# Performance work log

Measured on AMD Instinct MI355X. Metric: run time of the kernel, lower is better.

## Reference

```python
import jax, jax.numpy as jnp
import numpy as np

N, M, ND, K = 80000, 150000, 10000, 27  # active voxels, 2D painted points, downscaled voxels, 3x3x3 kernel
C3, C2, CP = 16, 64, 259                # 3D ch (stage 1), 2D conv ch, painted 2D feature ch
CM, CO = C3 + C2, 32 + 64               # mixed ch (80), downscale out ch (96)


def subm_conv(feats, nbr, W):
    """Submanifold sparse conv as gather + per-offset GEMM.
    feats: [N_in, Cin], nbr: [N_out, K] int (-1 = missing), W: [K, Cin, Cout]."""
    out = jnp.zeros((nbr.shape[0], W.shape[-1]), feats.dtype)
    for k in range(W.shape[0]):  # fixed small kernel loop (27)
        idx = nbr[:, k]
        g = jnp.where((idx >= 0)[:, None], feats[jnp.clip(idx, 0)], 0.0)
        out = out + g @ W[k]
    return out


def bn_relu(x, gamma, beta):  # folded eval-mode BN1d + ReLU
    return jax.nn.relu(x * gamma + beta)


def setup_inputs() -> dict:
    key = jax.random.key(0)
    ks = jax.random.split(key, 24)

    def w(k, shape, fan_in):
        return jax.random.normal(k, shape, jnp.float32) * (1.0 / np.sqrt(fan_in))

    inp = {
        'x3d': jax.random.normal(ks[0], (N, C3), jnp.float32),
        'f2d': jax.random.normal(ks[1], (M, CP), jnp.float32),
        'nn_idx': jax.random.randint(ks[2], (N,), -1, M, jnp.int32),     # -1 = no 2D match
        'nbr': jax.random.randint(ks[3], (N, K), -1, N, jnp.int32),      # -1 = missing neighbor
        'nbr_ds': jax.random.randint(ks[4], (ND, K), -1, N, jnp.int32),
        'W3d': w(ks[5], (K, C3, C3), K * C3),
        'g3d': jnp.ones((C3,), jnp.float32), 'b3d': jnp.zeros((C3,), jnp.float32),
        'Wg': w(ks[6], (C3, CP), C3), 'bg': jnp.zeros((CP,), jnp.float32),
        'Wc': w(ks[7], (C3, CP), C3), 'bc': jnp.zeros((CP,), jnp.float32),
        'Wp': w(ks[8], (CP, C2), CP),
        'W2d': w(ks[9], (K, C2, C2), K * C2),
        'g2d': jnp.ones((C2,), jnp.float32), 'b2d': jnp.zeros((C2,), jnp.float32),
        'Wm1': w(ks[10], (K, CM, CM), K * CM),
        'gm1': jnp.ones((CM,), jnp.float32), 'bm1': jnp.zeros((CM,), jnp.float32),
        'Wm2': w(ks[11], (K, CM, CM), K * CM),
        'gm2': jnp.ones((CM,), jnp.float32), 'bm2': jnp.zeros((CM,), jnp.float32),
        'Wa1': w(ks[12], (K, CM, CM), K * CM),
        'ga1': jnp.ones((CM,), jnp.float32), 'ba1': jnp.zeros((CM,), jnp.float32),
        'Wa2': w(ks[13], (K, CM, CM), K * CM),
        'ga2': jnp.ones((CM,), jnp.float32), 'ba2': jnp.zeros((CM,), jnp.float32),
        'Wds': w(ks[14], (K, CM, CO), K * CM),
        'gds': jnp.ones((CO,), jnp.float32), 'bds': jnp.zeros((CO,), jnp.float32),
    }
    return inp


def reference(x3d, f2d, nn_idx, nbr, nbr_ds,
              W3d, g3d, b3d, Wg, bg, Wc, bc, Wp,
              W2d, g2d, b2d,
              Wm1, gm1, bm1, Wm2, gm2, bm2,
              Wa1, ga1, ba1, Wa2, ga2, ba2,
              Wds, gds, bds):
    # irregular gather of painted 2D features to voxel sites (NN index, -1 invalid)
    f2g = jnp.where((nn_idx >= 0)[:, None], f2d[jnp.clip(nn_idx, 0)], 0.0)  # [N, 259]

    # 3D branch: SubMConv3d(C3->C3) + BN + ReLU
    y3d = bn_relu(subm_conv(x3d, nbr, W3d), g3d, b3d)                       # [N, 16]

    # per-stage gate / cross-gate (Linear + ReLU) on 3D features, applied to raw 2D feats
    gate = jax.nn.relu(y3d @ Wg + bg)                                       # [N, 259]
    cross = jax.nn.relu(y3d @ Wc + bc)                                      # [N, 259]

    # gated 2D branch: project gated painted feats to 64, SubMConv3d + BN + ReLU
    p2d = (gate * f2g) @ Wp                                                 # [N, 64]
    x2d = bn_relu(subm_conv(p2d, nbr, W2d), g2d, b2d)                       # [N, 64]
    cross2d = (cross * f2g) @ Wp                                            # [N, 64]

    # cross-modal mix + SparseBasicBlock (residual, two subm convs)
    mix = jnp.concatenate([y3d, x2d + cross2d], axis=-1)                    # [N, 80]
    h = bn_relu(subm_conv(mix, nbr, Wm1), gm1, bm1)
    h = jax.nn.relu(subm_conv(h, nbr, Wm2) * gm2 + bm2 + mix)

    # aggregation SparseBasicBlock
    a = bn_relu(subm_conv(h, nbr, Wa1), ga1, ba1)
    a = jax.nn.relu(subm_conv(a, nbr, Wa2) * ga2 + ba2 + h)

    # strided SparseConv3d downscale (gather from input sites at new out sites)
    out = bn_relu(subm_conv(a, nbr_ds, Wds), gds, bds)                      # [ND, 96]
    return out
```

## Files before the change

### kernel.cpp

```cpp
#include <hip/hip_runtime.h>

#define NPTS 80000
#define MPTS 150000
#define NDPTS 10000
#define KOFF 27
#define C3 16
#define CP 259
#define C2 64
#define CM 80
#define CO 96

typedef __attribute__((ext_vector_type(8))) short short8;
typedef __attribute__((ext_vector_type(4))) float f32x4;

__device__ inline short bf16r(float f) {
  union { float f; unsigned u; } x{f};
  unsigned r = (x.u + 0x7fffu + ((x.u >> 16) & 1u)) >> 16;
  return (short)r;
}

__global__ void wfrag_kernel(const float* __restrict__ W, short* __restrict__ WbfF,
                             int CIN, int COUT_, int KC) {
  const int NT = COUT_ / 16;
  int i = blockIdx.x * 256 + threadIdx.x;
  int total = KOFF * KC * NT * 512;
  if (i >= total) return;
  int j = i & 7, lane = (i >> 3) & 63;
  int rest = i >> 9;
  int t = rest % NT; rest /= NT;
  int q = rest % KC;
  int k = rest / KC;
  int ci = q * 32 + (lane >> 4) * 8 + j;
  int n = t * 16 + (lane & 15);
  float v = (ci < CIN) ? W[((size_t)k * CIN + ci) * COUT_ + n] : 0.f;
  WbfF[i] = bf16r(v);
}

__global__ void wpfrag_kernel(const float* __restrict__ Wp, short* __restrict__ WpF) {
  int i = blockIdx.x * 256 + threadIdx.x;
  if (i >= 9 * 4 * 64 * 8) return;
  int j = i & 7, lane = (i >> 3) & 63, t = (i >> 9) & 3, q = i >> 11;
  int k = q * 32 + (lane >> 4) * 8 + j;
  int n = t * 16 + (lane & 15);
  WpF[i] = (k < CP) ? bf16r(Wp[(size_t)k * C2 + n]) : (short)0;
}

__global__ __launch_bounds__(256) void conv3d_bnrelu_kernel(
    const float* __restrict__ x3d, const int* __restrict__ nbr,
    const float* __restrict__ W3d, const float* __restrict__ g3d,
    const float* __restrict__ b3d, float* __restrict__ y3d,
    float* __restrict__ mix, short* __restrict__ mixbf)
{
  __shared__ float wS[KOFF * C3 * C3];
  __shared__ float fS[16][C3];
  const int tid = threadIdx.x;
  const int base = blockIdx.x * 16;
  for (int e = tid; e < KOFF * C3 * C3; e += 256) wS[e] = W3d[e];
  const int r = tid >> 4, c = tid & 15;
  const int row = base + r;
  float acc = 0.f;
  for (int k = 0; k < KOFF; ++k) {
    int idx = nbr[row * KOFF + k];
    float fv = (idx >= 0) ? x3d[idx * C3 + c] : 0.f;
    __syncthreads();
    fS[r][c] = fv;
    __syncthreads();
    const float* wk = &wS[k * C3 * C3];
    #pragma unroll
    for (int ci = 0; ci < C3; ++ci)
      acc = fmaf(fS[r][ci], wk[ci * C3 + c], acc);
  }
  float v = fmaxf(fmaf(acc, g3d[c], b3d[c]), 0.f);
  y3d[row * C3 + c] = v;
  mix[row * CM + c] = v;
  mixbf[row * CM + c] = bf16r(v);
}

__global__ __launch_bounds__(256) void gate_cross_mfma_kernel(
    const float* __restrict__ y3d, const float* __restrict__ f2d,
    const int* __restrict__ nn_idx,
    const float* __restrict__ Wg, const float* __restrict__ bg,
    const float* __restrict__ Wc, const float* __restrict__ bc,
    const short* __restrict__ WpF,
    short* __restrict__ p2dbf, float* __restrict__ cross2d)
{
  constexpr int RS = 296;
  __shared__ short g1S[32 * RS];
  __shared__ short g2S[32 * RS];
  __shared__ float yS[32][C3];
  const int tid = threadIdx.x;
  const int lane = tid & 63;
  const int w = tid >> 6;
  const int lm = lane & 15;
  const int quad = lane >> 4;
  const int base = blockIdx.x * 32;

  for (int e = tid; e < 32 * 32; e += 256) {
    int r = e >> 5, cc = 256 + (e & 31);
    if (cc >= CP) {
      g1S[r * RS + cc] = 0;
      g2S[r * RS + cc] = 0;
    }
  }

  int ix[32];
  #pragma unroll
  for (int r = 0; r < 32; ++r) ix[r] = nn_idx[base + r];

  const int c = tid;
  float f[32];
  #pragma unroll
  for (int r = 0; r < 32; ++r)
    f[r] = (ix[r] >= 0) ? f2d[(size_t)ix[r] * CP + c] : 0.f;

  float ftail = 0.f;
  int tr = 0, tcc = 0;
  if (tid < 96) {
    tr = tid / 3; tcc = tid - tr * 3;
    if (ix[tr] >= 0) ftail = f2d[(size_t)ix[tr] * CP + 256 + tcc];
  }

  for (int e = tid; e < 32 * C3; e += 256)
    ((float*)yS)[e] = y3d[(size_t)base * C3 + e];

  float wg[16], wc[16];
  #pragma unroll
  for (int ci = 0; ci < 16; ++ci) {
    wg[ci] = Wg[ci * CP + c];
    wc[ci] = Wc[ci * CP + c];
  }
  const float bgv = bg[c], bcv = bc[c];

  __syncthreads();

  #pragma unroll
  for (int r = 0; r < 32; ++r) {
    float a1 = bgv, a2 = bcv;
    #pragma unroll
    for (int ci = 0; ci < 16; ++ci) {
      float yv = yS[r][ci];
      a1 = fmaf(yv, wg[ci], a1);
      a2 = fmaf(yv, wc[ci], a2);
    }
    g1S[r * RS + c] = bf16r(fmaxf(a1, 0.f) * f[r]);
    g2S[r * RS + c] = bf16r(fmaxf(a2, 0.f) * f[r]);
  }

  if (tid < 96) {
    const int c2 = 256 + tcc;
    float a1 = bg[c2], a2 = bc[c2];
    #pragma unroll
    for (int ci = 0; ci < 16; ++ci) {
      float yv = yS[tr][ci];
      a1 = fmaf(yv, Wg[ci * CP + c2], a1);
      a2 = fmaf(yv, Wc[ci * CP + c2], a2);
    }
    g1S[tr * RS + c2] = bf16r(fmaxf(a1, 0.f) * ftail);
    g2S[tr * RS + c2] = bf16r(fmaxf(a2, 0.f) * ftail);
  }
  __syncthreads();

  const int gsel = w & 1;
  const int mt = w >> 1;
  const short* gS = gsel ? g2S : g1S;
  f32x4 acc[4];
  #pragma unroll
  for (int t = 0; t < 4; ++t) {
    f32x4 z = {0.f, 0.f, 0.f, 0.f};
    acc[t] = z;
  }
  #pragma unroll
  for (int q = 0; q < 9; ++q) {
    short8 af = *(const short8*)&gS[(mt * 16 + lm) * RS + q * 32 + quad * 8];
    #pragma unroll
    for (int t = 0; t < 4; ++t) {
      short8 bf = *(const short8*)&WpF[(((q * 4 + t) * 64) + lane) * 8];
      acc[t] = __builtin_amdgcn_mfma_f32_16x16x32_bf16(af, bf, acc[t], 0, 0, 0);
    }
  }
  #pragma unroll
  for (int t = 0; t < 4; ++t) {
    const int cc = t * 16 + lm;
    #pragma unroll
    for (int rg = 0; rg < 4; ++rg) {
      const int row = base + mt * 16 + quad * 4 + rg;
      float v = acc[t][rg];
      if (gsel == 0)
        p2dbf[(size_t)row * C2 + cc] = bf16r(v);
      else
        cross2d[(size_t)row * C2 + cc] = v;
    }
  }
}

template <int CIN, int COUT_, int MODE, int MT>
__global__ __launch_bounds__(64, 2) void conv_nolds_kernel(
    const short* __restrict__ finbf, const int* __restrict__ nbr, int nrows,
    const short* __restrict__ WbfF, const float* __restrict__ gamma,
    const float* __restrict__ beta, const float* __restrict__ resf,
    float* __restrict__ outf, short* __restrict__ outbf)
{
  constexpr int KC = (CIN + 31) / 32;
  constexpr int DCH = CIN / 8;
  constexpr int NT = COUT_ / 16;

  const int lane = threadIdx.x;
  const int lm = lane & 15;
  const int quad = lane >> 4;
  const int base = blockIdx.x * (MT * 16);

  int rrow[MT];
  bool rok[MT];
  #pragma unroll
  for (int i = 0; i < MT; ++i) {
    rrow[i] = base + i * 16 + lm;
    rok[i] = rrow[i] < nrows;
  }

  f32x4 acc[MT][NT];
  #pragma unroll
  for (int i = 0; i < MT; ++i)
    #pragma unroll
    for (int t = 0; t < NT; ++t) {
      f32x4 z = {0.f, 0.f, 0.f, 0.f};
      acc[i][t] = z;
    }

  const short8 zero8 = {0, 0, 0, 0, 0, 0, 0, 0};

  auto loadIdx = [&](int (&id)[MT], int k) {
    #pragma unroll
    for (int i = 0; i < MT; ++i)
      id[i] = (k < KOFF && rok[i]) ? nbr[(size_t)rrow[i] * KOFF + k] : -1;
  };

  auto loadA = [&](short8 (&pa)[MT][KC], const int (&id)[MT]) {
    #pragma unroll
    for (int i = 0; i < MT; ++i) {
      const int safe = (id[i] < 0) ? 0 : id[i];
      const bool ok = id[i] >= 0;
      const short* src = finbf + (size_t)safe * CIN;
      #pragma unroll
      for (int q = 0; q < KC; ++q) {
        const int ch = q * 4 + quad;
        short8 v = zero8;
        if (ch < DCH) v = *(const short8*)(src + ch * 8);
        pa[i][q] = ok ? v : zero8;
      }
    }
  };

  auto computeK = [&](const short8 (&pa)[MT][KC], int k) {
    const short* wb = WbfF + ((size_t)k * KC * NT) * 512 + lane * 8;
    #pragma unroll
    for (int q = 0; q < KC; ++q) {
      #pragma unroll
      for (int t = 0; t < NT; ++t) {
        short8 bfr = *(const short8*)(wb + (q * NT + t) * 512);
        #pragma unroll
        for (int i = 0; i < MT; ++i)
          acc[i][t] = __builtin_amdgcn_mfma_f32_16x16x32_bf16(pa[i][q], bfr,
                                                              acc[i][t], 0, 0, 0);
      }
    }
  };

  int ia[MT], ib[MT], ic[MT];
  short8 paA[MT][KC], paB[MT][KC], paC[MT][KC];

  loadIdx(ia, 0); loadIdx(ib, 1); loadIdx(ic, 2);
  loadA(paA, ia); loadIdx(ia, 3);
  loadA(paB, ib); loadIdx(ib, 4);

  for (int kk = 0; kk < KOFF; kk += 3) {
    loadA(paC, ic); loadIdx(ic, kk + 5);
    computeK(paA, kk);
    loadA(paA, ia); loadIdx(ia, kk + 6);
    computeK(paB, kk + 1);
    loadA(paB, ib); loadIdx(ib, kk + 7);
    computeK(paC, kk + 2);
  }

  #pragma unroll
  for (int i = 0; i < MT; ++i) {
    int rbase = base + i * 16 + quad * 4;
    #pragma unroll
    for (int t = 0; t < NT; ++t) {
      int cc = t * 16 + lm;
      float g = gamma[cc], b = beta[cc];
      #pragma unroll
      for (int rg = 0; rg < 4; ++rg) {
        int row = rbase + rg;
        if (row >= nrows) continue;
        float v = acc[i][t][rg];
        if (MODE == 0) {
          outf[(size_t)row * COUT_ + cc] = fmaxf(fmaf(v, g, b), 0.f);
        } else if (MODE == 1) {
          outbf[(size_t)row * COUT_ + cc] = bf16r(fmaxf(fmaf(v, g, b), 0.f));
        } else if (MODE == 2) {
          float o = fmaxf(fmaf(v, g, b), 0.f) + resf[(size_t)row * C2 + cc];
          outf[(size_t)row * CM + 16 + cc] = o;
          outbf[(size_t)row * CM + 16 + cc] = bf16r(o);
        } else if (MODE == 3) {
          float o = fmaxf(fmaf(v, g, b) + resf[(size_t)row * COUT_ + cc], 0.f);
          outf[(size_t)row * COUT_ + cc] = o;
          outbf[(size_t)row * COUT_ + cc] = bf16r(o);
        } else {
          float o = fmaxf(fmaf(v, g, b) + resf[(size_t)row * COUT_ + cc], 0.f);
          outbf[(size_t)row * COUT_ + cc] = bf16r(o);
        }
      }
    }
  }
}

extern "C" void kernel_launch(void* const* d_in, const int* in_sizes, int n_in,
                              void* d_out, int out_size, void* d_ws, size_t ws_size,
                              hipStream_t stream) {
  const float* x3d  = (const float*)d_in[0];
  const float* f2d  = (const float*)d_in[1];
  const int*   nn   = (const int*)d_in[2];
  const int*   nbr  = (const int*)d_in[3];
  const int*   nbds = (const int*)d_in[4];
  const float* W3d  = (const float*)d_in[5];
  const float* g3d  = (const float*)d_in[6];
  const float* b3d  = (const float*)d_in[7];
  const float* Wg   = (const float*)d_in[8];
  const float* bg   = (const float*)d_in[9];
  const float* Wc   = (const float*)d_in[10];
  const float* bc   = (const float*)d_in[11];
  const float* Wp   = (const float*)d_in[12];
  const float* W2d  = (const float*)d_in[13];
  const float* g2d  = (const float*)d_in[14];
  const float* b2d  = (const float*)d_in[15];
  const float* Wm1  = (const float*)d_in[16];
  const float* gm1  = (const float*)d_in[17];
  const float* bm1  = (const float*)d_in[18];
  const float* Wm2  = (const float*)d_in[19];
  const float* gm2  = (const float*)d_in[20];
  const float* bm2  = (const float*)d_in[21];
  const float* Wa1  = (const float*)d_in[22];
  const float* ga1  = (const float*)d_in[23];
  const float* ba1  = (const float*)d_in[24];
  const float* Wa2  = (const float*)d_in[25];
  const float* ga2  = (const float*)d_in[26];
  const float* ba2  = (const float*)d_in[27];
  const float* Wds  = (const float*)d_in[28];
  const float* gds  = (const float*)d_in[29];
  const float* bds  = (const float*)d_in[30];

  const size_t N = NPTS;
  float* ws = (float*)d_ws;
  float* y3d     = ws;
  short* p2dbf   = (short*)(ws + N * 16);
  float* cross2d = ws + N * 48;
  float* mix     = ws + N * 112;
  short* mixbf   = (short*)(ws + N * 192);
  short* tmp1bf  = (short*)(ws + N * 232);
  float* hbuf    = ws + N * 272;
  short* hbufbf  = (short*)(ws + N * 352);
  short* abufbf  = (short*)ws;
  short* wtail  = (short*)(ws + N * 392);
  short* WbfF2d = wtail;
  short* WbfFm1 = WbfF2d + 110592;
  short* WbfFm2 = WbfFm1 + 207360;
  short* WbfFa1 = WbfFm2 + 207360;
  short* WbfFa2 = WbfFa1 + 207360;
  short* WbfFds = WbfFa2 + 207360;
  short* WpF    = WbfFds + 248832;

  wfrag_kernel<<<(110592 + 255) / 256, 256, 0, stream>>>(W2d, WbfF2d, 64, 64, 2);
  wfrag_kernel<<<(207360 + 255) / 256, 256, 0, stream>>>(Wm1, WbfFm1, 80, 80, 3);
  wfrag_kernel<<<(207360 + 255) / 256, 256, 0, stream>>>(Wm2, WbfFm2, 80, 80, 3);
  wfrag_kernel<<<(207360 + 255) / 256, 256, 0, stream>>>(Wa1, WbfFa1, 80, 80, 3);
  wfrag_kernel<<<(207360 + 255) / 256, 256, 0, stream>>>(Wa2, WbfFa2, 80, 80, 3);
  wfrag_kernel<<<(248832 + 255) / 256, 256, 0, stream>>>(Wds, WbfFds, 80, 96, 3);
  wpfrag_kernel<<<(9 * 4 * 64 * 8 + 255) / 256, 256, 0, stream>>>(Wp, WpF);

  conv3d_bnrelu_kernel<<<NPTS / 16, 256, 0, stream>>>(x3d, nbr, W3d, g3d, b3d,
                                                      y3d, mix, mixbf);
  gate_cross_mfma_kernel<<<NPTS / 32, 256, 0, stream>>>(y3d, f2d, nn, Wg, bg,
                                                        Wc, bc, WpF, p2dbf,
                                                        cross2d);

  const int gridM2 = (NPTS + 31) / 32;
  const int gridM4 = (NPTS + 63) / 64;
  conv_nolds_kernel<64, 64, 2, 2><<<gridM2, 64, 0, stream>>>(
      p2dbf, nbr, NPTS, WbfF2d, g2d, b2d, cross2d, mix, mixbf);
  conv_nolds_kernel<80, 80, 1, 2><<<gridM2, 64, 0, stream>>>(
      mixbf, nbr, NPTS, WbfFm1, gm1, bm1, nullptr, nullptr, tmp1bf);
  conv_nolds_kernel<80, 80, 3, 4><<<gridM4, 64, 0, stream>>>(
      tmp1bf, nbr, NPTS, WbfFm2, gm2, bm2, mix, hbuf, hbufbf);
  conv_nolds_kernel<80, 80, 1, 2><<<gridM2, 64, 0, stream>>>(
      hbufbf, nbr, NPTS, WbfFa1, ga1, ba1, nullptr, nullptr, tmp1bf);
  conv_nolds_kernel<80, 80, 4, 2><<<gridM2, 64, 0, stream>>>(
      tmp1bf, nbr, NPTS, WbfFa2, ga2, ba2, hbuf, nullptr, abufbf);

  const int gridDS = (NDPTS + 31) / 32;
  conv_nolds_kernel<80, 96, 0, 2><<<gridDS, 64, 0, stream>>>(
      abufbf, nbds, NDPTS, WbfFds, gds, bds, nullptr, (float*)d_out, nullptr);
}
```

Measured before the change: 1.161 ms.

## Stage sparse-conv gathers and weights into LDS via async global_load_lds double buffering

Replaces the register-prefetch sparse conv kernel with one that preloads the block's neighbor indices into shared memory and streams gathered feature rows and weight fragments into double-buffered LDS using global_load_lds, synchronised with manual vmcnt waits. The goal is to hide gather latency behind MFMA work and cut register pressure without tying up VGPRs for prefetched fragments. The tile is fixed at 32 rows (the MT=4 variant is dropped) and launch bounds change to one block per SIMD hint. The hand-coded vmcnt thresholds are brittle and depend on the exact number of outstanding loads, and the launch bounds limit occupancy.

```diff
diff --git a/kernel.cpp b/kernel.cpp
--- a/kernel.cpp
+++ b/kernel.cpp
@@ -17,6 +17,12 @@
   union { float f; unsigned u; } x{f};
   unsigned r = (x.u + 0x7fffu + ((x.u >> 16) & 1u)) >> 16;
   return (short)r;
+}
+
+typedef __attribute__((address_space(1))) const unsigned int g_u32;
+typedef __attribute__((address_space(3))) unsigned int l_u32;
+__device__ __forceinline__ void gload_lds16(const void* g, void* l) {
+  __builtin_amdgcn_global_load_lds((g_u32*)g, (l_u32*)l, 16, 0, 0);
 }
 
 __global__ void wfrag_kernel(const float* __restrict__ W, short* __restrict__ WbfF,
@@ -193,8 +199,8 @@
   }
 }
 
-template <int CIN, int COUT_, int MODE, int MT>
-__global__ __launch_bounds__(64, 2) void conv_nolds_kernel(
+template <int CIN, int COUT_, int MODE>
+__global__ __launch_bounds__(64, 1) void conv_glds_kernel(
     const short* __restrict__ finbf, const int* __restrict__ nbr, int nrows,
     const short* __restrict__ WbfF, const float* __restrict__ gamma,
     const float* __restrict__ beta, const float* __restrict__ resf,
@@ -203,18 +209,22 @@
   constexpr int KC = (CIN + 31) / 32;
   constexpr int DCH = CIN / 8;
   constexpr int NT = COUT_ / 16;
+  constexpr int MT = 2;
+  constexpr int WN = MT * KC + KC * NT;
+
+  __shared__ short8 aS[2 * MT * KC * 64];
+  __shared__ short8 bS[2 * KC * NT * 64];
+  __shared__ int nbrS[32 * KOFF];
 
   const int lane = threadIdx.x;
   const int lm = lane & 15;
   const int quad = lane >> 4;
-  const int base = blockIdx.x * (MT * 16);
-
-  int rrow[MT];
-  bool rok[MT];
-  #pragma unroll
-  for (int i = 0; i < MT; ++i) {
-    rrow[i] = base + i * 16 + lm;
-    rok[i] = rrow[i] < nrows;
+  const int base = blockIdx.x * 32;
+
+  for (int e = lane; e < 32 * KOFF; e += 64) {
+    int r = e / KOFF;
+    int row = base + r;
+    nbrS[e] = (row < nrows) ? nbr[(size_t)row * KOFF + (e - r * KOFF)] : -1;
   }
 
   f32x4 acc[MT][NT];
@@ -226,59 +236,125 @@
       acc[i][t] = z;
     }
 
-  const short8 zero8 = {0, 0, 0, 0, 0, 0, 0, 0};
-
-  auto loadIdx = [&](int (&id)[MT], int k) {
+  auto readIdx = [&](int k, int (&id)[MT]) {
     #pragma unroll
     for (int i = 0; i < MT; ++i)
-      id[i] = (k < KOFF && rok[i]) ? nbr[(size_t)rrow[i] * KOFF + k] : -1;
+      id[i] = (k < KOFF) ? nbrS[(i * 16 + lm) * KOFF + k] : -1;
   };
 
-  auto loadA = [&](short8 (&pa)[MT][KC], const int (&id)[MT]) {
+  auto stage = [&](int k2, const int (&id)[MT]) {
+    const int slot = k2 & 1;
     #pragma unroll
     for (int i = 0; i < MT; ++i) {
       const int safe = (id[i] < 0) ? 0 : id[i];
-      const bool ok = id[i] >= 0;
-      const short* src = finbf + (size_t)safe * CIN;
+      const short* srow = finbf + (size_t)safe * CIN;
       #pragma unroll
       for (int q = 0; q < KC; ++q) {
         const int ch = q * 4 + quad;
-        short8 v = zero8;
-        if (ch < DCH) v = *(const short8*)(src + ch * 8);
-        pa[i][q] = ok ? v : zero8;
+        const int chs = (ch < DCH) ? ch : (DCH - 1);
+        gload_lds16(srow + chs * 8, &aS[((slot * MT + i) * KC + q) * 64]);
       }
     }
+    const short* wb = WbfF + (size_t)k2 * (KC * NT * 512) + lane * 8;
+    #pragma unroll
+    for (int q = 0; q < KC; ++q)
+      #pragma unroll
+      for (int t = 0; t < NT; ++t)
+        gload_lds16(wb + (q * NT + t) * 512, &bS[((slot * KC + q) * NT + t) * 64]);
   };
 
-  auto computeK = [&](const short8 (&pa)[MT][KC], int k) {
-    const short* wb = WbfF + ((size_t)k * KC * NT) * 512 + lane * 8;
-    #pragma unroll
-    for (int q = 0; q < KC; ++q) {
-      #pragma unroll
-      for (int t = 0; t < NT; ++t) {
-        short8 bfr = *(const short8*)(wb + (q * NT + t) * 512);
+  auto waitSlot = [&]() {
+    if constexpr (WN == 12)      asm volatile("s_waitcnt vmcnt(12)" ::: "memory");
+    else if constexpr (WN == 21) asm volatile("s_waitcnt vmcnt(21)" ::: "memory");
+    else                         asm volatile("s_waitcnt vmcnt(24)" ::: "memory");
+  };
+
+  const short8 zero8 = {0, 0, 0, 0, 0, 0, 0, 0};
+
+  {
+    int id0[MT], id1[MT];
+    readIdx(0, id0);
+    readIdx(1, id1);
+    stage(0, id0);
+    stage(1, id1);
+  }
+
+  for (int k = 0; k < KOFF - 1; ++k) {
+    const int slot = k & 1;
+    waitSlot();
+    short8 va[MT][KC];
+    #pragma unroll
+    for (int i = 0; i < MT; ++i)
+      #pragma unroll
+      for (int q = 0; q < KC; ++q)
+        va[i][q] = aS[((slot * MT + i) * KC + q) * 64 + lane];
+    short8 vb[KC][NT];
+    #pragma unroll
+    for (int q = 0; q < KC; ++q)
+      #pragma unroll
+      for (int t = 0; t < NT; ++t)
+        vb[q][t] = bS[((slot * KC + q) * NT + t) * 64 + lane];
+    int ikc[MT], ikn[MT];
+    readIdx(k, ikc);
+    readIdx(k + 2, ikn);
+    asm volatile("s_waitcnt lgkmcnt(0)" ::: "memory");
+    __builtin_amdgcn_sched_barrier(0);
+    #pragma unroll
+    for (int i = 0; i < MT; ++i) {
+      const bool okr = ikc[i] >= 0;
+      #pragma unroll
+      for (int q = 0; q < KC; ++q) {
+        const bool okc = okr && ((q * 4 + quad) < DCH);
+        va[i][q] = okc ? va[i][q] : zero8;
+      }
+    }
+    if (k + 2 < KOFF) stage(k + 2, ikn);
+    #pragma unroll
+    for (int q = 0; q < KC; ++q)
+      #pragma unroll
+      for (int t = 0; t < NT; ++t)
         #pragma unroll
         for (int i = 0; i < MT; ++i)
-          acc[i][t] = __builtin_amdgcn_mfma_f32_16x16x32_bf16(pa[i][q], bfr,
+          acc[i][t] = __builtin_amdgcn_mfma_f32_16x16x32_bf16(va[i][q], vb[q][t],
                                                               acc[i][t], 0, 0, 0);
+  }
+  {
+    const int k = KOFF - 1;
+    const int slot = k & 1;
+    asm volatile("s_waitcnt vmcnt(0)" ::: "memory");
+    short8 va[MT][KC];
+    #pragma unroll
+    for (int i = 0; i < MT; ++i)
+      #pragma unroll
+      for (int q = 0; q < KC; ++q)
+        va[i][q] = aS[((slot * MT + i) * KC + q) * 64 + lane];
+    short8 vb[KC][NT];
+    #pragma unroll
+    for (int q = 0; q < KC; ++q)
+      #pragma unroll
+      for (int t = 0; t < NT; ++t)
+        vb[q][t] = bS[((slot * KC + q) * NT + t) * 64 + lane];
+    int ikc[MT];
+    readIdx(k, ikc);
+    asm volatile("s_waitcnt lgkmcnt(0)" ::: "memory");
+    __builtin_amdgcn_sched_barrier(0);
+    #pragma unroll
+    for (int i = 0; i < MT; ++i) {
+      const bool okr = ikc[i] >= 0;
+      #pragma unroll
+      for (int q = 0; q < KC; ++q) {
+        const bool okc = okr && ((q * 4 + quad) < DCH);
+        va[i][q] = okc ? va[i][q] : zero8;
       }
     }
-  };
-
-  int ia[MT], ib[MT], ic[MT];
-  short8 paA[MT][KC], paB[MT][KC], paC[MT][KC];
-
-  loadIdx(ia, 0); loadIdx(ib, 1); loadIdx(ic, 2);
-  loadA(paA, ia); loadIdx(ia, 3);
-  loadA(paB, ib); loadIdx(ib, 4);
-
-  for (int kk = 0; kk < KOFF; kk += 3) {
-    loadA(paC, ic); loadIdx(ic, kk + 5);
-    computeK(paA, kk);
-    loadA(paA, ia); loadIdx(ia, kk + 6);
-    computeK(paB, kk + 1);
-    loadA(paB, ib); loadIdx(ib, kk + 7);
-    computeK(paC, kk + 2);
+    #pragma unroll
+    for (int q = 0; q < KC; ++q)
+      #pragma unroll
+      for (int t = 0; t < NT; ++t)
+        #pragma unroll
+        for (int i = 0; i < MT; ++i)
+          acc[i][t] = __builtin_amdgcn_mfma_f32_16x16x32_bf16(va[i][q], vb[q][t],
+                                                              acc[i][t], 0, 0, 0);
   }
 
   #pragma unroll
@@ -383,20 +459,19 @@
                                                         Wc, bc, WpF, p2dbf,
                                                         cross2d);
 
-  const int gridM2 = (NPTS + 31) / 32;
-  const int gridM4 = (NPTS + 63) / 64;
-  conv_nolds_kernel<64, 64, 2, 2><<<gridM2, 64, 0, stream>>>(
+  const int gridW = (NPTS + 31) / 32;
+  conv_glds_kernel<64, 64, 2><<<gridW, 64, 0, stream>>>(
       p2dbf, nbr, NPTS, WbfF2d, g2d, b2d, cross2d, mix, mixbf);
-  conv_nolds_kernel<80, 80, 1, 2><<<gridM2, 64, 0, stream>>>(
+  conv_glds_kernel<80, 80, 1><<<gridW, 64, 0, stream>>>(
       mixbf, nbr, NPTS, WbfFm1, gm1, bm1, nullptr, nullptr, tmp1bf);
-  conv_nolds_kernel<80, 80, 3, 4><<<gridM4, 64, 0, stream>>>(
+  conv_glds_kernel<80, 80, 3><<<gridW, 64, 0, stream>>>(
       tmp1bf, nbr, NPTS, WbfFm2, gm2, bm2, mix, hbuf, hbufbf);
-  conv_nolds_kernel<80, 80, 1, 2><<<gridM2, 64, 0, stream>>>(
+  conv_glds_kernel<80, 80, 1><<<gridW, 64, 0, stream>>>(
       hbufbf, nbr, NPTS, WbfFa1, ga1, ba1, nullptr, nullptr, tmp1bf);
-  conv_nolds_kernel<80, 80, 4, 2><<<gridM2, 64, 0, stream>>>(
+  conv_glds_kernel<80, 80, 4><<<gridW, 64, 0, stream>>>(
       tmp1bf, nbr, NPTS, WbfFa2, ga2, ba2, hbuf, nullptr, abufbf);
 
   const int gridDS = (NDPTS + 31) / 32;
-  conv_nolds_kernel<80, 96, 0, 2><<<gridDS, 64, 0, stream>>>(
+  conv_glds_kernel<80, 96, 0><<<gridDS, 64, 0, stream>>>(
       abufbf, nbds, NDPTS, WbfFds, gds, bds, nullptr, (float*)d_out, nullptr);
 }
```

After: 1.093 ms. -5.8%, faster.
